# Kernel optimization log

Measured on AMD Instinct MI355X. Metric: run time of the kernel, lower is better.

The kernel has to match this reference:

```python
import jax, jax.numpy as jnp
import numpy as np

D_MODEL = 1024
N_HEADS = 16
D_K = D_MODEL // N_HEADS
B, T = 4, 2048


def setup_inputs() -> dict:
    key = jax.random.key(0)
    ks = jax.random.split(key, 6)
    scale = 1.0 / np.sqrt(D_MODEL)
    q = jax.random.normal(ks[0], (B, T, D_MODEL), dtype=jnp.float32)
    # causal mask: True = masked / ignored (upper triangle)
    causal = jnp.triu(jnp.ones((T, T), dtype=bool), k=1)
    mask = jnp.broadcast_to(causal, (B, 1, T, T))
    Wq = jax.random.normal(ks[1], (D_MODEL, D_MODEL), dtype=jnp.float32) * scale
    Wk = jax.random.normal(ks[2], (D_MODEL, D_MODEL), dtype=jnp.float32) * scale
    Wv = jax.random.normal(ks[3], (D_MODEL, D_MODEL), dtype=jnp.float32) * scale
    Wo = jax.random.normal(ks[4], (D_MODEL, D_MODEL), dtype=jnp.float32) * scale
    bq = jnp.zeros((D_MODEL,), jnp.float32)
    bk = jnp.zeros((D_MODEL,), jnp.float32)
    bv = jnp.zeros((D_MODEL,), jnp.float32)
    bo = jnp.zeros((D_MODEL,), jnp.float32)
    return {"q": q, "mask": mask, "Wq": Wq, "bq": bq, "Wk": Wk, "bk": bk,
            "Wv": Wv, "bv": bv, "Wo": Wo, "bo": bo}


def reference(q, mask, Wq, bq, Wk, bk, Wv, bv, Wo, bo):
    # Self-attention: k = v = q (module defaults). Weights stored torch-style
    # (out, in): y = x @ W.T + b.
    b, tq, _ = q.shape
    qh = (q @ Wq.T + bq).reshape(b, tq, N_HEADS, D_K).transpose(0, 2, 1, 3)  # (B,H,T,dk)
    kh = (q @ Wk.T + bk).reshape(b, tq, N_HEADS, D_K).transpose(0, 2, 1, 3)
    vh = (q @ Wv.T + bv).reshape(b, tq, N_HEADS, D_K).transpose(0, 2, 1, 3)
    attn = jnp.einsum('bhqd,bhkd->bhqk', qh, kh) / np.sqrt(D_K).astype(np.float32)
    attn = jnp.where(mask, -jnp.inf, attn)
    attn = jax.nn.softmax(attn, axis=-1)
    out = jnp.einsum('bhqk,bhkd->bhqd', attn, vh)
    out = out.transpose(0, 2, 1, 3).reshape(b, tq, D_MODEL)
    return out @ Wo.T + bo
```

## Files before the change

### kernel.cpp

```cpp
#include <hip/hip_runtime.h>
#include <hip/hip_bf16.h>
#include <stdint.h>

#define D_MODEL 1024
#define NH      16
#define DKH     64
#define BATCH   4
#define SEQ     2048
#define MROWS   (BATCH*SEQ)

typedef __hip_bfloat16 bf16;
typedef __attribute__((ext_vector_type(8))) short  bf16x8;
typedef __attribute__((ext_vector_type(4))) short  bf16x4;
typedef __attribute__((ext_vector_type(4))) float  f32x4;
typedef __attribute__((ext_vector_type(2))) unsigned int u32x2;

#define CEXP 0.18033688011112042f

__device__ __forceinline__ bf16 f2bf(float x){ return __float2bfloat16(x); }

__device__ __forceinline__ void gload_lds16(const void* g, void* l) {
  __builtin_amdgcn_global_load_lds(
      (const __attribute__((address_space(1))) unsigned int*)g,
      (__attribute__((address_space(3))) unsigned int*)l, 16, 0, 0);
}

__device__ __forceinline__ unsigned int cvtpk(float lo, float hi) {
  unsigned int r;
  asm("v_cvt_pk_bf16_f32 %0, %1, %2" : "=v"(r) : "v"(lo), "v"(hi));
  return r;
}

__global__ __launch_bounds__(256)
void cvt_all(const float* __restrict__ q,
             const float* __restrict__ w0, const float* __restrict__ w1,
             const float* __restrict__ w2, const float* __restrict__ w3,
             bf16* __restrict__ qdst, bf16* __restrict__ wdst)
{
  const int NQB = (MROWS * D_MODEL) / 1024;
  const int bid = blockIdx.x;
  const float* src;
  bf16* dst;
  int i;
  if (bid < NQB) {
    src = q; dst = qdst;
    i = bid * 1024 + threadIdx.x * 4;
  } else {
    const int b2 = bid - NQB;
    const int w = b2 >> 10;
    src = (w == 0) ? w0 : (w == 1) ? w1 : (w == 2) ? w2 : w3;
    dst = wdst + (size_t)w * (D_MODEL * D_MODEL);
    i = (b2 & 1023) * 1024 + threadIdx.x * 4;
  }
  f32x4 v = *(const f32x4*)&src[i];
  union { bf16 e[4]; bf16x4 v4; } u;
  u.e[0] = f2bf(v[0]); u.e[1] = f2bf(v[1]);
  u.e[2] = f2bf(v[2]); u.e[3] = f2bf(v[3]);
  *(bf16x4*)&dst[i] = u.v4;
}

template <int MODE>
__global__ __launch_bounds__(512, 2)
void gemm8(const bf16* __restrict__ A, const bf16* __restrict__ W,
           const float* __restrict__ b0, const float* __restrict__ b1,
           const float* __restrict__ b2, void* __restrict__ Cbase)
{
  constexpr int K    = D_MODEL;
  constexpr int NT   = K / 64;
  constexpr int SLOT = (128 + 256) * 64;
  __shared__ __align__(16) short ring[3 * SLOT];

  const int tid  = threadIdx.x;
  const int lane = tid & 63;
  const int wave = tid >> 6;
  const int lm   = lane & 15;
  const int quad = lane >> 4;
  const int wm   = (wave >> 2) * 64;
  const int wn   = (wave & 3) * 64;
  const int bm   = blockIdx.x * 128;
  const int bn   = blockIdx.y * 256;

  const int rr    = tid >> 3;
  const int kperm = ((tid & 7) ^ (rr & 7)) * 8;
  const bf16* aS0 = A + (int64_t)(bm + rr) * K + kperm;
  const bf16* aS1 = aS0 + (int64_t)64 * K;
  const bf16* bS0 = W + (int64_t)(bn + rr) * K + kperm;
  const bf16* bS1 = bS0 + (int64_t)64 * K;
  const bf16* bS2 = bS0 + (int64_t)128 * K;
  const bf16* bS3 = bS0 + (int64_t)192 * K;

  f32x4 acc[4][4] = {};

#define STAGE8(T, S)                                                          \
  do {                                                                        \
    const int k0_ = (T) * 64;                                                 \
    short* As_ = &ring[(S) * SLOT];                                           \
    short* Bs_ = As_ + 128 * 64;                                              \
    gload_lds16(aS0 + k0_, &As_[tid * 8]);                                    \
    gload_lds16(aS1 + k0_, &As_[(tid + 512) * 8]);                            \
    gload_lds16(bS0 + k0_, &Bs_[tid * 8]);                                    \
    gload_lds16(bS1 + k0_, &Bs_[(tid + 512) * 8]);                            \
    gload_lds16(bS2 + k0_, &Bs_[(tid + 1024) * 8]);                           \
    gload_lds16(bS3 + k0_, &Bs_[(tid + 1536) * 8]);                           \
  } while (0)

  STAGE8(0, 0);
  STAGE8(1, 1);

#pragma unroll
  for (int t = 0; t < NT; ++t) {
    if (t < NT - 1) asm volatile("s_waitcnt vmcnt(6)" ::: "memory");
    else            asm volatile("s_waitcnt vmcnt(0)" ::: "memory");
    __builtin_amdgcn_s_barrier();
    asm volatile("" ::: "memory");

    const short* As = &ring[(t % 3) * SLOT];
    const short* Bs = As + 128 * 64;
    short* Ad = &ring[((t + 2) % 3) * SLOT];
    short* Bd = Ad + 128 * 64;
    const bool dost = (t + 2 < NT);
    const int k2 = (t + 2) * 64;

#pragma unroll
    for (int kk = 0; kk < 2; ++kk) {
      bf16x8 af[4], bfr[4];
#pragma unroll
      for (int i = 0; i < 4; ++i) {
        const int ra = wm + i * 16 + lm;
        af[i]  = *(const bf16x8*)&As[ra * 64 + (((kk * 4 + quad) ^ (ra & 7))) * 8];
        const int rb = wn + i * 16 + lm;
        bfr[i] = *(const bf16x8*)&Bs[rb * 64 + (((kk * 4 + quad) ^ (rb & 7))) * 8];
      }
      if (dost) {
        if (kk == 0) {
          gload_lds16(aS0 + k2, &Ad[tid * 8]);
          gload_lds16(aS1 + k2, &Ad[(tid + 512) * 8]);
          gload_lds16(bS0 + k2, &Bd[tid * 8]);
        } else {
          gload_lds16(bS1 + k2, &Bd[(tid + 512) * 8]);
          gload_lds16(bS2 + k2, &Bd[(tid + 1024) * 8]);
          gload_lds16(bS3 + k2, &Bd[(tid + 1536) * 8]);
        }
      }
      __builtin_amdgcn_s_barrier();
      asm volatile("s_waitcnt lgkmcnt(0)" ::: "memory");
      __builtin_amdgcn_sched_barrier(0);
      __builtin_amdgcn_s_setprio(1);
#pragma unroll
      for (int i = 0; i < 4; ++i)
#pragma unroll
        for (int j = 0; j < 4; ++j)
          acc[i][j] = __builtin_amdgcn_mfma_f32_16x16x32_bf16(af[i], bfr[j], acc[i][j], 0, 0, 0);
      __builtin_amdgcn_s_setprio(0);
    }
  }
#undef STAGE8

  if constexpr (MODE == 1) {
    float* Cp = (float*)Cbase;
#pragma unroll
    for (int j = 0; j < 4; ++j) {
      const int n = bn + wn + j * 16 + lm;
      const float bv = b0[n];
#pragma unroll
      for (int i = 0; i < 4; ++i)
#pragma unroll
        for (int r = 0; r < 4; ++r) {
          const int m = bm + wm + i * 16 + quad * 4 + r;
          Cp[(int64_t)m * D_MODEL + n] = acc[i][j][r] + bv;
        }
    }
  } else {
    const int proj = bn >> 10;
    const int nl0  = bn & 1023;
    const float* bias = (proj == 0) ? b0 : (proj == 1) ? b1 : b2;
    if (proj == 2) {
      bf16* Vt = (bf16*)Cbase + 2 * (size_t)MROWS * D_MODEL;
#pragma unroll
      for (int j = 0; j < 4; ++j) {
        const int nl = nl0 + wn + j * 16 + lm;
        const float bv = bias[nl];
#pragma unroll
        for (int i = 0; i < 4; ++i) {
          const int m0 = bm + wm + i * 16 + quad * 4;
          const int t0 = m0 & 2047;
          const int j64 = t0 & 63;
          const int pos = (((j64 >> 5) * 4 + ((j64 >> 2) & 3)) << 3)
                        + (((j64 >> 4) & 1) << 2);
          const int64_t base = (int64_t)((m0 >> 11) * 16 + (nl >> 6)) * (DKH * SEQ)
                             + (nl & 63) * SEQ + (t0 & ~63) + pos;
          union { bf16 e[4]; bf16x4 v4; } u;
#pragma unroll
          for (int r = 0; r < 4; ++r) u.e[r] = f2bf(acc[i][j][r] + bv);
          *(bf16x4*)&Vt[base] = u.v4;
        }
      }
    } else {
      bf16* Cp = (bf16*)Cbase + (size_t)proj * MROWS * D_MODEL;
      const float sc = (proj == 0) ? CEXP : 1.0f;
#pragma unroll
      for (int j = 0; j < 4; ++j) {
        const int nl = nl0 + wn + j * 16 + lm;
        const float bv = bias[nl];
#pragma unroll
        for (int i = 0; i < 4; ++i)
#pragma unroll
          for (int r = 0; r < 4; ++r) {
            const int m = bm + wm + i * 16 + quad * 4 + r;
            Cp[(int64_t)m * D_MODEL + nl] = f2bf((acc[i][j][r] + bv) * sc);
          }
      }
    }
  }
}

__global__ __launch_bounds__(256)
void attn_causal(const bf16* __restrict__ Q, const bf16* __restrict__ Kg,
                 const bf16* __restrict__ Vt, bf16* __restrict__ O)
{
  __shared__ __align__(16) short lK[2][64 * 64];
  __shared__ __align__(16) short lV[2][64 * 64];

  const int bid  = blockIdx.x;
  const int qt   = 31 - (bid >> 6);
  const int bh   = bid & 63;

  const int tid  = threadIdx.x;
  const int lane = tid & 63;
  const int wave = tid >> 6;
  const int lm   = lane & 15;
  const int quad = lane >> 4;
  const int qbase = qt * 64;
  const int64_t qkbase = (int64_t)((bh >> 4) * SEQ) * D_MODEL + (bh & 15) * DKH;
  const bf16* Kbase = Kg + qkbase;
  const bf16* Vbase = Vt + (int64_t)bh * DKH * SEQ;

  bf16x8 qf[2];
  {
    const bf16* qrow = Q + qkbase + (int64_t)(qbase + wave * 16 + lm) * D_MODEL;
    qf[0] = *(const bf16x8*)&qrow[quad * 8];
    qf[1] = *(const bf16x8*)&qrow[32 + quad * 8];
  }

  f32x4 o_acc[4] = {};
  f32x4 o_sum   = {};
  const bf16x8 ones8 = {16256, 16256, 16256, 16256,
                        16256, 16256, 16256, 16256};

  const int srow = tid >> 3;
  const int sg   = (tid & 7) ^ (srow & 7);
  const int wqv  = wave * 16 + lm;

  const bf16* kp0 = Kbase + (int64_t)srow        * D_MODEL + sg * 8;
  const bf16* kp1 = Kbase + (int64_t)(srow + 32) * D_MODEL + sg * 8;
  const bf16* vp0 = Vbase + (int64_t)srow        * SEQ + sg * 8;
  const bf16* vp1 = Vbase + (int64_t)(srow + 32) * SEQ + sg * 8;

#define STAGE(KB, BUF)                                                        \
  do {                                                                        \
    gload_lds16(kp0 + (int64_t)(KB) * D_MODEL, &lK[BUF][tid * 8]);            \
    gload_lds16(kp1 + (int64_t)(KB) * D_MODEL, &lK[BUF][(tid + 256) * 8]);    \
    gload_lds16(vp0 + (KB), &lV[BUF][tid * 8]);                               \
    gload_lds16(vp1 + (KB), &lV[BUF][(tid + 256) * 8]);                       \
  } while (0)

  STAGE(0, 0);

  for (int kt = 0; kt <= qt; ++kt) {
    const int cur = kt & 1;
    __syncthreads();
    if (kt < qt) STAGE((kt + 1) * 64, cur ^ 1);

    const short* lKc = lK[cur];
    const short* lVc = lV[cur];

    f32x4 s[4];
    __builtin_amdgcn_s_setprio(1);
#pragma unroll
    for (int ni = 0; ni < 4; ++ni) {
      const int row = ni * 16 + lm;
      f32x4 zz = {};
      bf16x8 k0 = *(const bf16x8*)&lKc[row * 64 + ((quad       ^ (row & 7))) * 8];
      bf16x8 k1 = *(const bf16x8*)&lKc[row * 64 + (((4 + quad) ^ (row & 7))) * 8];
      zz = __builtin_amdgcn_mfma_f32_16x16x32_bf16(k0, qf[0], zz, 0, 0, 0);
      zz = __builtin_amdgcn_mfma_f32_16x16x32_bf16(k1, qf[1], zz, 0, 0, 0);
      s[ni] = zz;
    }
    __builtin_amdgcn_s_setprio(0);

    if (kt == qt) {
#pragma unroll
      for (int ni = 0; ni < 4; ++ni) {
        const int kp = ni * 16 + quad * 4;
#pragma unroll
        for (int r = 0; r < 4; ++r)
          if (kp + r > wqv) s[ni][r] = -1e30f;
      }
    }

    unsigned int pku[4][2];
#pragma unroll
    for (int ni = 0; ni < 4; ++ni) {
      const float p0 = __builtin_amdgcn_exp2f(s[ni][0]);
      const float p1 = __builtin_amdgcn_exp2f(s[ni][1]);
      const float p2 = __builtin_amdgcn_exp2f(s[ni][2]);
      const float p3 = __builtin_amdgcn_exp2f(s[ni][3]);
      pku[ni][0] = cvtpk(p0, p1);
      pku[ni][1] = cvtpk(p2, p3);
    }

    __builtin_amdgcn_s_setprio(1);
#pragma unroll
    for (int m = 0; m < 2; ++m) {
      union { unsigned int u[4]; bf16x8 v; } au;
      au.u[0] = pku[2 * m][0];     au.u[1] = pku[2 * m][1];
      au.u[2] = pku[2 * m + 1][0]; au.u[3] = pku[2 * m + 1][1];
      o_sum = __builtin_amdgcn_mfma_f32_16x16x32_bf16(au.v, ones8, o_sum, 0, 0, 0);
#pragma unroll
      for (int di = 0; di < 4; ++di) {
        const int vrow = di * 16 + lm;
        const bf16x8 vb = *(const bf16x8*)&lVc[vrow * 64
            + (((m * 4 + quad) ^ (vrow & 7))) * 8];
        o_acc[di] = __builtin_amdgcn_mfma_f32_16x16x32_bf16(au.v, vb, o_acc[di], 0, 0, 0);
      }
    }
    __builtin_amdgcn_s_setprio(0);
  }
#undef STAGE

  float lr[4];
#pragma unroll
  for (int r = 0; r < 4; ++r) lr[r] = 1.0f / o_sum[r];

#pragma unroll
  for (int di = 0; di < 4; ++di)
#pragma unroll
    for (int r = 0; r < 4; ++r) {
      const int qrow = qbase + wave * 16 + quad * 4 + r;
      O[qkbase + (int64_t)qrow * D_MODEL + di * 16 + lm] = f2bf(o_acc[di][r] * lr[r]);
    }
}

extern "C" void kernel_launch(void* const* d_in, const int* in_sizes, int n_in,
                              void* d_out, int out_size, void* d_ws, size_t ws_size,
                              hipStream_t stream)
{
  const float* q  = (const float*)d_in[0];
  const float* Wq = (const float*)d_in[2];
  const float* bq = (const float*)d_in[3];
  const float* Wk = (const float*)d_in[4];
  const float* bk = (const float*)d_in[5];
  const float* Wv = (const float*)d_in[6];
  const float* bv = (const float*)d_in[7];
  const float* Wo = (const float*)d_in[8];
  const float* bo = (const float*)d_in[9];
  float* out = (float*)d_out;

  const size_t NQ = (size_t)MROWS * D_MODEL;
  const size_t NW = (size_t)D_MODEL * D_MODEL;

  bf16* qb  = (bf16*)d_ws;
  bf16* Wb  = qb + NQ;
  bf16* Qw  = Wb + 4 * NW;
  bf16* Kw  = Qw + NQ;
  bf16* Vtw = Kw + NQ;

  cvt_all<<<dim3(NQ / 1024 + 4 * NW / 1024), 256, 0, stream>>>(
      q, Wq, Wk, Wv, Wo, qb, Wb);

  gemm8<0><<<dim3(MROWS / 128, 3 * D_MODEL / 256), 512, 0, stream>>>(
      qb, Wb, bq, bk, bv, Qw);

  attn_causal<<<dim3(BATCH * NH * (SEQ / 64)), 256, 0, stream>>>(Qw, Kw, Vtw, qb);

  gemm8<1><<<dim3(MROWS / 128, D_MODEL / 256), 512, 0, stream>>>(
      qb, Wb + 3 * NW, bo, bo, bo, out);
}
```

Baseline: 255.4 us.

## Fuse fp32-to-bf16 conversion and QKV GEMM into one persistent cooperative kernel

Replaces the separate conversion kernel and the QKV projection GEMM with one cooperative kernel of 256 persistent blocks. Each block first converts a grid-strided slice of the input and weights to bf16, then waits on a grid-wide sync, then computes three 128x256 output tiles in sequence. This removes one kernel launch and the launch gap between the two stages. In exchange it relies on grid sync and cooperative launch, caps occupancy at one 512-thread block per CU with no tail overlap, and serialises the conversion phase against the GEMM.

Result: slower. 406.1 us (+59.0%).

```diff
diff --git a/kernel.cpp b/kernel.cpp
--- a/kernel.cpp
+++ b/kernel.cpp
@@ -1,6 +1,9 @@
 #include <hip/hip_runtime.h>
+#include <hip/hip_cooperative_groups.h>
 #include <hip/hip_bf16.h>
 #include <stdint.h>
+
+namespace cg = cooperative_groups;
 
 #define D_MODEL 1024
 #define NH      16
@@ -31,32 +34,178 @@
   return r;
 }
 
-__global__ __launch_bounds__(256)
-void cvt_all(const float* __restrict__ q,
-             const float* __restrict__ w0, const float* __restrict__ w1,
-             const float* __restrict__ w2, const float* __restrict__ w3,
-             bf16* __restrict__ qdst, bf16* __restrict__ wdst)
-{
-  const int NQB = (MROWS * D_MODEL) / 1024;
-  const int bid = blockIdx.x;
-  const float* src;
-  bf16* dst;
-  int i;
-  if (bid < NQB) {
-    src = q; dst = qdst;
-    i = bid * 1024 + threadIdx.x * 4;
-  } else {
-    const int b2 = bid - NQB;
-    const int w = b2 >> 10;
-    src = (w == 0) ? w0 : (w == 1) ? w1 : (w == 2) ? w2 : w3;
-    dst = wdst + (size_t)w * (D_MODEL * D_MODEL);
-    i = (b2 & 1023) * 1024 + threadIdx.x * 4;
-  }
+__device__ __forceinline__ void cvt4(const float* src, bf16* dst, int i) {
   f32x4 v = *(const f32x4*)&src[i];
   union { bf16 e[4]; bf16x4 v4; } u;
   u.e[0] = f2bf(v[0]); u.e[1] = f2bf(v[1]);
   u.e[2] = f2bf(v[2]); u.e[3] = f2bf(v[3]);
   *(bf16x4*)&dst[i] = u.v4;
+}
+
+__global__ __launch_bounds__(512, 1)
+void qkv_fused(const float* __restrict__ q,
+               const float* __restrict__ Wqf, const float* __restrict__ Wkf,
+               const float* __restrict__ Wvf, const float* __restrict__ Wof,
+               const float* __restrict__ b0, const float* __restrict__ b1,
+               const float* __restrict__ b2,
+               bf16* __restrict__ qb, bf16* __restrict__ Wb,
+               bf16* __restrict__ Cbase)
+{
+  constexpr int K    = D_MODEL;
+  constexpr int NT   = K / 64;
+  constexpr int SLOT = (128 + 256) * 64;
+  constexpr int NQ4  = (MROWS * D_MODEL) / 4;
+  constexpr int NW4  = (D_MODEL * D_MODEL) / 4;
+  __shared__ __align__(16) short ring[3 * SLOT];
+
+  {
+    const int gtid = blockIdx.x * 512 + threadIdx.x;
+    for (int i = gtid; i < NQ4; i += 256 * 512) cvt4(q, qb, i * 4);
+    const float* ws[4] = { Wqf, Wkf, Wvf, Wof };
+#pragma unroll
+    for (int w = 0; w < 4; ++w) {
+      bf16* wd = Wb + (size_t)w * (D_MODEL * D_MODEL);
+      for (int i = gtid; i < NW4; i += 256 * 512) cvt4(ws[w], wd, i * 4);
+    }
+  }
+  __threadfence();
+  cg::this_grid().sync();
+  __threadfence();
+
+  const int tid  = threadIdx.x;
+  const int lane = tid & 63;
+  const int wave = tid >> 6;
+  const int lm   = lane & 15;
+  const int quad = lane >> 4;
+  const int wm   = (wave >> 2) * 64;
+  const int wn   = (wave & 3) * 64;
+  const int bm   = (blockIdx.x & 63) * 128;
+  const int g3   = (blockIdx.x >> 6) * 3;
+
+  const int rr    = tid >> 3;
+  const int kperm = ((tid & 7) ^ (rr & 7)) * 8;
+  const bf16* aS0 = qb + (int64_t)(bm + rr) * K + kperm;
+  const bf16* aS1 = aS0 + (int64_t)64 * K;
+
+  for (int tt = 0; tt < 3; ++tt) {
+    const int bnIdx = g3 + tt;
+    const int bn    = bnIdx * 256;
+    const bf16* bS0 = Wb + (int64_t)(bn + rr) * K + kperm;
+    const bf16* bS1 = bS0 + (int64_t)64 * K;
+    const bf16* bS2 = bS0 + (int64_t)128 * K;
+    const bf16* bS3 = bS0 + (int64_t)192 * K;
+
+    asm volatile("s_waitcnt vmcnt(0)" ::: "memory");
+    __syncthreads();
+
+    f32x4 acc[4][4] = {};
+
+#define STAGE8(T, S)                                                          \
+    do {                                                                      \
+      const int k0_ = (T) * 64;                                               \
+      short* As_ = &ring[(S) * SLOT];                                         \
+      short* Bs_ = As_ + 128 * 64;                                            \
+      gload_lds16(aS0 + k0_, &As_[tid * 8]);                                  \
+      gload_lds16(aS1 + k0_, &As_[(tid + 512) * 8]);                          \
+      gload_lds16(bS0 + k0_, &Bs_[tid * 8]);                                  \
+      gload_lds16(bS1 + k0_, &Bs_[(tid + 512) * 8]);                          \
+      gload_lds16(bS2 + k0_, &Bs_[(tid + 1024) * 8]);                         \
+      gload_lds16(bS3 + k0_, &Bs_[(tid + 1536) * 8]);                         \
+    } while (0)
+
+    STAGE8(0, 0);
+    STAGE8(1, 1);
+
+#pragma unroll
+    for (int t = 0; t < NT; ++t) {
+      if (t < NT - 1) asm volatile("s_waitcnt vmcnt(6)" ::: "memory");
+      else            asm volatile("s_waitcnt vmcnt(0)" ::: "memory");
+      __builtin_amdgcn_s_barrier();
+      asm volatile("" ::: "memory");
+
+      const short* As = &ring[(t % 3) * SLOT];
+      const short* Bs = As + 128 * 64;
+      short* Ad = &ring[((t + 2) % 3) * SLOT];
+      short* Bd = Ad + 128 * 64;
+      const bool dost = (t + 2 < NT);
+      const int k2 = (t + 2) * 64;
+
+#pragma unroll
+      for (int kk = 0; kk < 2; ++kk) {
+        bf16x8 af[4], bfr[4];
+#pragma unroll
+        for (int i = 0; i < 4; ++i) {
+          const int ra = wm + i * 16 + lm;
+          af[i]  = *(const bf16x8*)&As[ra * 64 + (((kk * 4 + quad) ^ (ra & 7))) * 8];
+          const int rb = wn + i * 16 + lm;
+          bfr[i] = *(const bf16x8*)&Bs[rb * 64 + (((kk * 4 + quad) ^ (rb & 7))) * 8];
+        }
+        if (dost) {
+          if (kk == 0) {
+            gload_lds16(aS0 + k2, &Ad[tid * 8]);
+            gload_lds16(aS1 + k2, &Ad[(tid + 512) * 8]);
+            gload_lds16(bS0 + k2, &Bd[tid * 8]);
+          } else {
+            gload_lds16(bS1 + k2, &Bd[(tid + 512) * 8]);
+            gload_lds16(bS2 + k2, &Bd[(tid + 1024) * 8]);
+            gload_lds16(bS3 + k2, &Bd[(tid + 1536) * 8]);
+          }
+        }
+        __builtin_amdgcn_s_barrier();
+        asm volatile("s_waitcnt lgkmcnt(0)" ::: "memory");
+        __builtin_amdgcn_sched_barrier(0);
+        __builtin_amdgcn_s_setprio(1);
+#pragma unroll
+        for (int i = 0; i < 4; ++i)
+#pragma unroll
+          for (int j = 0; j < 4; ++j)
+            acc[i][j] = __builtin_amdgcn_mfma_f32_16x16x32_bf16(af[i], bfr[j], acc[i][j], 0, 0, 0);
+        __builtin_amdgcn_s_setprio(0);
+      }
+    }
+#undef STAGE8
+
+    const int proj = bn >> 10;
+    const int nl0  = bn & 1023;
+    const float* bias = (proj == 0) ? b0 : (proj == 1) ? b1 : b2;
+    if (proj == 2) {
+      bf16* Vt = Cbase + 2 * (size_t)MROWS * D_MODEL;
+#pragma unroll
+      for (int j = 0; j < 4; ++j) {
+        const int nl = nl0 + wn + j * 16 + lm;
+        const float bv = bias[nl];
+#pragma unroll
+        for (int i = 0; i < 4; ++i) {
+          const int m0 = bm + wm + i * 16 + quad * 4;
+          const int t0 = m0 & 2047;
+          const int j64 = t0 & 63;
+          const int pos = (((j64 >> 5) * 4 + ((j64 >> 2) & 3)) << 3)
+                        + (((j64 >> 4) & 1) << 2);
+          const int64_t base = (int64_t)((m0 >> 11) * 16 + (nl >> 6)) * (DKH * SEQ)
+                             + (nl & 63) * SEQ + (t0 & ~63) + pos;
+          union { bf16 e[4]; bf16x4 v4; } u;
+#pragma unroll
+          for (int r = 0; r < 4; ++r) u.e[r] = f2bf(acc[i][j][r] + bv);
+          *(bf16x4*)&Vt[base] = u.v4;
+        }
+      }
+    } else {
+      bf16* Cp = Cbase + (size_t)proj * MROWS * D_MODEL;
+      const float sc = (proj == 0) ? CEXP : 1.0f;
+#pragma unroll
+      for (int j = 0; j < 4; ++j) {
+        const int nl = nl0 + wn + j * 16 + lm;
+        const float bv = bias[nl];
+#pragma unroll
+        for (int i = 0; i < 4; ++i)
+#pragma unroll
+          for (int r = 0; r < 4; ++r) {
+            const int m = bm + wm + i * 16 + quad * 4 + r;
+            Cp[(int64_t)m * D_MODEL + nl] = f2bf((acc[i][j][r] + bv) * sc);
+          }
+      }
+    }
+  }
 }
 
 template <int MODE>
@@ -170,47 +319,6 @@
           Cp[(int64_t)m * D_MODEL + n] = acc[i][j][r] + bv;
         }
     }
-  } else {
-    const int proj = bn >> 10;
-    const int nl0  = bn & 1023;
-    const float* bias = (proj == 0) ? b0 : (proj == 1) ? b1 : b2;
-    if (proj == 2) {
-      bf16* Vt = (bf16*)Cbase + 2 * (size_t)MROWS * D_MODEL;
-#pragma unroll
-      for (int j = 0; j < 4; ++j) {
-        const int nl = nl0 + wn + j * 16 + lm;
-        const float bv = bias[nl];
-#pragma unroll
-        for (int i = 0; i < 4; ++i) {
-          const int m0 = bm + wm + i * 16 + quad * 4;
-          const int t0 = m0 & 2047;
-          const int j64 = t0 & 63;
-          const int pos = (((j64 >> 5) * 4 + ((j64 >> 2) & 3)) << 3)
-                        + (((j64 >> 4) & 1) << 2);
-          const int64_t base = (int64_t)((m0 >> 11) * 16 + (nl >> 6)) * (DKH * SEQ)
-                             + (nl & 63) * SEQ + (t0 & ~63) + pos;
-          union { bf16 e[4]; bf16x4 v4; } u;
-#pragma unroll
-          for (int r = 0; r < 4; ++r) u.e[r] = f2bf(acc[i][j][r] + bv);
-          *(bf16x4*)&Vt[base] = u.v4;
-        }
-      }
-    } else {
-      bf16* Cp = (bf16*)Cbase + (size_t)proj * MROWS * D_MODEL;
-      const float sc = (proj == 0) ? CEXP : 1.0f;
-#pragma unroll
-      for (int j = 0; j < 4; ++j) {
-        const int nl = nl0 + wn + j * 16 + lm;
-        const float bv = bias[nl];
-#pragma unroll
-        for (int i = 0; i < 4; ++i)
-#pragma unroll
-          for (int r = 0; r < 4; ++r) {
-            const int m = bm + wm + i * 16 + quad * 4 + r;
-            Cp[(int64_t)m * D_MODEL + nl] = f2bf((acc[i][j][r] + bv) * sc);
-          }
-      }
-    }
   }
 }
 
@@ -291,10 +399,10 @@
     if (kt == qt) {
 #pragma unroll
       for (int ni = 0; ni < 4; ++ni) {
-        const int kp = ni * 16 + quad * 4;
+        const int kp_ = ni * 16 + quad * 4;
 #pragma unroll
         for (int r = 0; r < 4; ++r)
-          if (kp + r > wqv) s[ni][r] = -1e30f;
+          if (kp_ + r > wqv) s[ni][r] = -1e30f;
       }
     }
 
@@ -365,11 +473,11 @@
   bf16* Kw  = Qw + NQ;
   bf16* Vtw = Kw + NQ;
 
-  cvt_all<<<dim3(NQ / 1024 + 4 * NW / 1024), 256, 0, stream>>>(
-      q, Wq, Wk, Wv, Wo, qb, Wb);
-
-  gemm8<0><<<dim3(MROWS / 128, 3 * D_MODEL / 256), 512, 0, stream>>>(
-      qb, Wb, bq, bk, bv, Qw);
+  void* args[] = { (void*)&q, (void*)&Wq, (void*)&Wk, (void*)&Wv, (void*)&Wo,
+                   (void*)&bq, (void*)&bk, (void*)&bv,
+                   (void*)&qb, (void*)&Wb, (void*)&Qw };
+  hipLaunchCooperativeKernel((const void*)qkv_fused, dim3(256), dim3(512),
+                             args, 0, stream);
 
   attn_causal<<<dim3(BATCH * NH * (SEQ / 64)), 256, 0, stream>>>(Qw, Kw, Vtw, qb);
 
```
